# Kernel optimization log

Hardware: AMD Instinct MI355X
Metric: run time of the kernel (lower is better)

The kernel has to match this reference:

```python
import jax, jax.numpy as jnp
import numpy as np

T, B, OBS, H, FC = 128, 512, 1024, 512, 512
LN_EPS = 1e-6  # flax LayerNorm default


def setup_inputs() -> dict:
    key = jax.random.key(0)
    ks = jax.random.split(key, 8)
    sc = lambda k, shape, s: jax.random.normal(k, shape, jnp.float32) * s
    return dict(
        hidden=jnp.zeros((B, H), jnp.float32),  # GRUCell.initialize_carry -> zeros
        world_state=jax.random.normal(ks[0], (T, B, OBS), jnp.float32),
        dones=jax.random.bernoulli(ks[1], 0.05, (T, B)),
        Wd=sc(ks[2], (OBS, H), 1.0 / np.sqrt(OBS)),
        bd=jnp.zeros((H,), jnp.float32),
        ln_scale=jnp.ones((H,), jnp.float32),
        ln_bias=jnp.zeros((H,), jnp.float32),
        Wi=sc(ks[3], (H, 3 * H), 1.0 / np.sqrt(H)),  # input-side GRU weights [r|z|n]
        bi=jnp.zeros((3 * H,), jnp.float32),
        Wh=sc(ks[4], (H, 3 * H), 1.0 / np.sqrt(H)),  # hidden-side GRU weights [r|z|n]
        bhn=jnp.zeros((H,), jnp.float32),            # flax GRU: only hn dense has bias
        Wc1=sc(ks[5], (H, FC), 1.0 / np.sqrt(H)),
        bc1=jnp.zeros((FC,), jnp.float32),
        Wc2=sc(ks[6], (FC, 1), 1.0 / np.sqrt(FC)),
        bc2=jnp.zeros((1,), jnp.float32),
    )


def reference(hidden, world_state, dones, Wd, bd, ln_scale, ln_bias,
              Wi, bi, Wh, bhn, Wc1, bc1, Wc2, bc2):
    # Embed: Dense -> relu -> LayerNorm, applied to all timesteps at once
    emb = jax.nn.relu(world_state @ Wd + bd)                      # [T,B,H]
    mu = emb.mean(-1, keepdims=True)
    var = ((emb - mu) ** 2).mean(-1, keepdims=True)
    emb = (emb - mu) * jax.lax.rsqrt(var + LN_EPS) * ln_scale + ln_bias

    # Precompute input-side GRU projections for all steps (hoisted out of scan)
    xproj = emb @ Wi + bi                                         # [T,B,3H]

    def step(h, inputs):
        xp, done = inputs
        h = jnp.where(done[:, None], 0.0, h)                      # reset carry on done
        xr, xz, xn = jnp.split(xp, 3, axis=-1)
        hr, hz, hn = jnp.split(h @ Wh, 3, axis=-1)                # [B,H] each
        r = jax.nn.sigmoid(xr + hr)
        z = jax.nn.sigmoid(xz + hz)
        n = jnp.tanh(xn + r * (hn + bhn))
        h_new = (1.0 - z) * n + z * h
        return h_new, h_new

    h_last, ys = jax.lax.scan(step, hidden, (xproj, dones))       # ys: [T,B,H]

    critic = jax.nn.relu(ys @ Wc1 + bc1)                          # [T,B,FC]
    value = jnp.squeeze(critic @ Wc2 + bc2, axis=-1)              # [T,B]
    return h_last, value
```

## Files before the change

### kernel.cpp

```cpp
#include <hip/hip_runtime.h>
#include <stdint.h>

#define T_STEPS 128
#define BATCH   512
#define OBSD    1024
#define HD      512
#define FCD     512
#define MROWS   (T_STEPS * BATCH)

typedef unsigned short ushort_t;
typedef __attribute__((ext_vector_type(8))) short bf16x8;
typedef __attribute__((ext_vector_type(4))) float f32x4;
typedef __attribute__((ext_vector_type(2))) uint32_t u32x2;

__device__ inline ushort_t f2bf(float f) {
    union { float f; uint32_t u; } v; v.f = f;
    uint32_t r = v.u + 0x7FFFu + ((v.u >> 16) & 1u);
    return (ushort_t)(r >> 16);
}
__device__ inline float bf2f(ushort_t h) {
    union { uint32_t u; float f; } v; v.u = ((uint32_t)h) << 16;
    return v.f;
}
__device__ inline float fsigmoid(float x) {
    x = fminf(fmaxf(x, -30.f), 30.f);
    return 1.f / (1.f + __expf(-x));
}
__device__ inline float ftanh(float x) {
    float e = __expf(fminf(fmaxf(2.f * x, -30.f), 30.f));
    return (e - 1.f) / (e + 1.f);
}
__device__ inline uint32_t cvt_pk_bf16(float lo, float hi) {
    uint32_t r;
    asm("v_cvt_pk_bf16_f32 %0, %1, %2" : "=v"(r) : "v"(lo), "v"(hi));
    return r;
}
__device__ inline void gload16(const void* g, void* l) {
    __builtin_amdgcn_global_load_lds(
        (const __attribute__((address_space(1))) uint32_t*)g,
        (__attribute__((address_space(3))) uint32_t*)l, 16, 0, 0);
}

__global__ void transpose_to_bf16(const float* __restrict__ in,
                                  ushort_t* __restrict__ out, int R, int C) {
    __shared__ float tile[32][33];
    int tx = threadIdx.x, ty = threadIdx.y;
    int c0 = blockIdx.x * 32, r0 = blockIdx.y * 32;
    for (int yy = 0; yy < 4; ++yy)
        tile[ty + 8 * yy][tx] = in[(size_t)(r0 + ty + 8 * yy) * C + c0 + tx];
    __syncthreads();
    for (int yy = 0; yy < 4; ++yy)
        out[(size_t)(c0 + ty + 8 * yy) * R + r0 + tx] = f2bf(tile[tx][ty + 8 * yy]);
}

__global__ void init_misc(float* __restrict__ v, const float* __restrict__ bc2,
                          unsigned* __restrict__ bar) {
    int i = blockIdx.x * blockDim.x + threadIdx.x;
    if (i < MROWS) v[i] = bc2[0];
    if (i < 2048) bar[i] = 0u;
}

template <int K, int EPI, bool AF32>
__global__ __launch_bounds__(256, 2) void gemm128(
    const void* __restrict__ Aptr, const ushort_t* __restrict__ BT,
    const float* __restrict__ bias, ushort_t* __restrict__ Cout, int ldc,
    const float* __restrict__ wc2, float* __restrict__ value) {
    __shared__ __align__(16) ushort_t Als[128][32];
    __shared__ __align__(16) ushort_t Bls[128][32];
    int tid = threadIdx.x;
    int wave = tid >> 6, lane = tid & 63, quad = lane >> 4, l16 = lane & 15;
    int wr = wave >> 1, wc = wave & 1;
    int bm = blockIdx.y * 128, bn = blockIdx.x * 128;

    f32x4 acc[4][4];
#pragma unroll
    for (int m = 0; m < 4; ++m)
#pragma unroll
        for (int n = 0; n < 4; ++n) acc[m][n] = (f32x4){0.f, 0.f, 0.f, 0.f};

    int srow = tid >> 2;
    int sk = (tid & 3) * 8;
    const ushort_t* Bt0 = &BT[(size_t)(bn + srow) * K + sk];
    const ushort_t* Bt1 = &BT[(size_t)(bn + 64 + srow) * K + sk];
    char* AlsDst = (char*)&Als[0][0] + tid * 16;
    char* BlsDst = (char*)&Bls[0][0] + tid * 16;
    const ushort_t* At0 = nullptr;
    const ushort_t* At1 = nullptr;
    if constexpr (!AF32) {
        const ushort_t* A = (const ushort_t*)Aptr;
        At0 = &A[(size_t)(bm + srow) * K + sk];
        At1 = &A[(size_t)(bm + 64 + srow) * K + sk];
    }

#pragma unroll 1
    for (int k0 = 0; k0 < K; k0 += 32) {
        if constexpr (AF32) {
            const float* A = (const float*)Aptr;
#pragma unroll
            for (int j = 0; j < 4; ++j) {
                int f = tid + 256 * j;
                int r = f >> 3, c4 = f & 7;
                float4 av =
                    *(const float4*)&A[(size_t)(bm + r) * K + k0 + c4 * 4];
                u32x2 w;
                w[0] = cvt_pk_bf16(av.x, av.y);
                w[1] = cvt_pk_bf16(av.z, av.w);
                *(u32x2*)&Als[r][c4 * 4] = w;
            }
        } else {
            gload16(At0 + k0, AlsDst);
            gload16(At1 + k0, AlsDst + 4096);
        }
        gload16(Bt0 + k0, BlsDst);
        gload16(Bt1 + k0, BlsDst + 4096);
        __syncthreads();

        bf16x8 af[4], bfr[4];
#pragma unroll
        for (int m = 0; m < 4; ++m)
            af[m] = *(const bf16x8*)&Als[wr * 64 + m * 16 + l16][quad * 8];
#pragma unroll
        for (int n = 0; n < 4; ++n)
            bfr[n] = *(const bf16x8*)&Bls[wc * 64 + n * 16 + l16][quad * 8];
#pragma unroll
        for (int m = 0; m < 4; ++m)
#pragma unroll
            for (int n = 0; n < 4; ++n)
                acc[m][n] = __builtin_amdgcn_mfma_f32_16x16x32_bf16(
                    af[m], bfr[n], acc[m][n], 0, 0, 0);
        __syncthreads();
    }

    int rbase = bm + wr * 64 + quad * 4;
    if constexpr (EPI == 0 || EPI == 1) {
#pragma unroll
        for (int n = 0; n < 4; ++n) {
            int col = bn + wc * 64 + n * 16 + l16;
            float bv = bias[col];
#pragma unroll
            for (int m = 0; m < 4; ++m) {
#pragma unroll
                for (int i = 0; i < 4; ++i) {
                    float v = acc[m][n][i] + bv;
                    if constexpr (EPI == 0) v = fmaxf(v, 0.f);
                    Cout[(size_t)(rbase + m * 16 + i) * ldc + col] = f2bf(v);
                }
            }
        }
    } else {
        float s[4][4];
#pragma unroll
        for (int m = 0; m < 4; ++m)
#pragma unroll
            for (int i = 0; i < 4; ++i) s[m][i] = 0.f;
#pragma unroll
        for (int n = 0; n < 4; ++n) {
            int col = bn + wc * 64 + n * 16 + l16;
            float bv = bias[col], w2 = wc2[col];
#pragma unroll
            for (int m = 0; m < 4; ++m)
#pragma unroll
                for (int i = 0; i < 4; ++i)
                    s[m][i] += fmaxf(acc[m][n][i] + bv, 0.f) * w2;
        }
#pragma unroll
        for (int m = 0; m < 4; ++m)
#pragma unroll
            for (int i = 0; i < 4; ++i) {
                float v = s[m][i];
                v += __shfl_xor(v, 1);
                v += __shfl_xor(v, 2);
                v += __shfl_xor(v, 4);
                v += __shfl_xor(v, 8);
                if (l16 == 0) atomicAdd(&value[rbase + m * 16 + i], v);
            }
    }
}

__global__ __launch_bounds__(256) void ln_kernel(ushort_t* __restrict__ emb,
                                                 const float* __restrict__ scale,
                                                 const float* __restrict__ biasv) {
    int wave = threadIdx.x >> 6, lane = threadIdx.x & 63;
    size_t row = (size_t)blockIdx.x * 4 + wave;
    ushort_t* p = &emb[row * HD + lane * 8];
    bf16x8 xv = *(const bf16x8*)p;
    float x[8];
    float sum = 0.f, sq = 0.f;
    for (int j = 0; j < 8; ++j) {
        x[j] = bf2f((ushort_t)xv[j]);
        sum += x[j];
        sq += x[j] * x[j];
    }
    for (int off = 32; off > 0; off >>= 1) {
        sum += __shfl_xor(sum, off);
        sq += __shfl_xor(sq, off);
    }
    float mean = sum * (1.f / 512.f);
    float var = fmaxf(sq * (1.f / 512.f) - mean * mean, 0.f);
    float inv = rsqrtf(var + 1e-6f);
    bf16x8 ov;
    for (int j = 0; j < 8; ++j) {
        int col = lane * 8 + j;
        ov[j] = (short)f2bf((x[j] - mean) * inv * scale[col] + biasv[col]);
    }
    *(bf16x8*)p = ov;
}

__global__ __launch_bounds__(256, 1) void scan_coop(
    const float* __restrict__ hidden, const int* __restrict__ dones,
    const ushort_t* __restrict__ WhT, const float* __restrict__ bhn,
    const ushort_t* __restrict__ xproj, ushort_t* __restrict__ ys,
    float* __restrict__ hlast, ushort_t* hb0, ushort_t* hb1,
    unsigned* bar) {
    __shared__ __align__(16) ushort_t Wls[48][520];
    int tid = threadIdx.x;
    int wave = tid >> 6, lane = tid & 63, quad = lane >> 4, l16 = lane & 15;
    int bid = blockIdx.x;
    int bg = bid & 7, cg = bid >> 3;
    int row0 = bg * 64 + wave * 16;
    int col0 = cg * 16;

    for (int idx = tid; idx < 48 * 64; idx += 256) {
        int c = idx >> 6, ck = (idx & 63) * 8;
        int g = c >> 4, lc = c & 15;
        *(bf16x8*)&Wls[c][ck] =
            *(const bf16x8*)&WhT[(size_t)(g * 512 + col0 + lc) * 512 + ck];
    }

    float mast[4];
    int rbase = row0 + quad * 4;
#pragma unroll
    for (int i = 0; i < 4; ++i) {
        float h0 = hidden[(size_t)(rbase + i) * HD + col0 + l16];
        mast[i] = dones[rbase + i] ? 0.f : h0;
    }
    float bhnv = bhn[col0 + l16];

    unsigned* cnt = &bar[bg * 256];
    unsigned* mycnt = &cnt[(cg & 7) * 32];

#pragma unroll
    for (int i = 0; i < 4; ++i) {
        unsigned u = f2bf(mast[i]);
        unsigned p1 = __shfl_xor((int)u, 1);
        unsigned u32 = u | (p1 << 16);
        unsigned hi = __shfl_xor((int)u32, 2);
        if ((l16 & 3) == 0) {
            unsigned long long q =
                (unsigned long long)u32 | ((unsigned long long)hi << 32);
            __hip_atomic_store(
                (unsigned long long*)&hb0[(size_t)(rbase + i) * HD + col0 + l16],
                q, __ATOMIC_RELAXED, __HIP_MEMORY_SCOPE_AGENT);
        }
    }
    float xr[4], xz[4], xn[4];
    int dn_nxt[4];
#pragma unroll
    for (int i = 0; i < 4; ++i) {
        size_t m = (size_t)(rbase + i);
        const ushort_t* xp = &xproj[m * 1536 + col0 + l16];
        xr[i] = bf2f(xp[0]);
        xz[i] = bf2f(xp[512]);
        xn[i] = bf2f(xp[1024]);
        dn_nxt[i] = dones[BATCH + rbase + i];
    }
    __builtin_amdgcn_s_waitcnt(0);
    __syncthreads();
    if (tid == 0)
        __hip_atomic_fetch_add(mycnt, 1u, __ATOMIC_RELAXED,
                               __HIP_MEMORY_SCOPE_AGENT);

    for (int t = 0; t < T_STEPS; ++t) {
        if (tid == 0) {
            unsigned target = 32u * (unsigned)(t + 1);
            for (;;) {
                unsigned s = 0;
#pragma unroll
                for (int c = 0; c < 8; ++c)
                    s += __hip_atomic_load(&cnt[c * 32], __ATOMIC_RELAXED,
                                           __HIP_MEMORY_SCOPE_AGENT);
                if (s >= target) break;
                __builtin_amdgcn_s_sleep(1);
            }
        }
        __syncthreads();
        asm volatile("" ::: "memory");
        ushort_t* rbuf = (t & 1) ? hb1 : hb0;
        ushort_t* wnext = (t & 1) ? hb0 : hb1;

        bf16x8 afr[16];
        {
            const ushort_t* ap =
                &rbuf[(size_t)(row0 + l16) * HD + quad * 8];
            asm volatile(
                "global_load_dwordx4 %0, %16, off sc0 sc1\n\t"
                "global_load_dwordx4 %1, %16, off offset:64 sc0 sc1\n\t"
                "global_load_dwordx4 %2, %16, off offset:128 sc0 sc1\n\t"
                "global_load_dwordx4 %3, %16, off offset:192 sc0 sc1\n\t"
                "global_load_dwordx4 %4, %16, off offset:256 sc0 sc1\n\t"
                "global_load_dwordx4 %5, %16, off offset:320 sc0 sc1\n\t"
                "global_load_dwordx4 %6, %16, off offset:384 sc0 sc1\n\t"
                "global_load_dwordx4 %7, %16, off offset:448 sc0 sc1\n\t"
                "global_load_dwordx4 %8, %16, off offset:512 sc0 sc1\n\t"
                "global_load_dwordx4 %9, %16, off offset:576 sc0 sc1\n\t"
                "global_load_dwordx4 %10, %16, off offset:640 sc0 sc1\n\t"
                "global_load_dwordx4 %11, %16, off offset:704 sc0 sc1\n\t"
                "global_load_dwordx4 %12, %16, off offset:768 sc0 sc1\n\t"
                "global_load_dwordx4 %13, %16, off offset:832 sc0 sc1\n\t"
                "global_load_dwordx4 %14, %16, off offset:896 sc0 sc1\n\t"
                "global_load_dwordx4 %15, %16, off offset:960 sc0 sc1\n\t"
                "s_waitcnt vmcnt(0)"
                : "=&v"(afr[0]), "=&v"(afr[1]), "=&v"(afr[2]), "=&v"(afr[3]),
                  "=&v"(afr[4]), "=&v"(afr[5]), "=&v"(afr[6]), "=&v"(afr[7]),
                  "=&v"(afr[8]), "=&v"(afr[9]), "=&v"(afr[10]), "=&v"(afr[11]),
                  "=&v"(afr[12]), "=&v"(afr[13]), "=&v"(afr[14]), "=&v"(afr[15])
                : "v"(ap)
                : "memory");
        }
        f32x4 aR = (f32x4){0.f, 0.f, 0.f, 0.f};
        f32x4 aZ = (f32x4){0.f, 0.f, 0.f, 0.f};
        f32x4 aN = (f32x4){0.f, 0.f, 0.f, 0.f};
#pragma unroll
        for (int kt = 0; kt < 16; ++kt) {
            bf16x8 bR = *(const bf16x8*)&Wls[l16][kt * 32 + quad * 8];
            bf16x8 bZ = *(const bf16x8*)&Wls[16 + l16][kt * 32 + quad * 8];
            bf16x8 bN = *(const bf16x8*)&Wls[32 + l16][kt * 32 + quad * 8];
            aR = __builtin_amdgcn_mfma_f32_16x16x32_bf16(afr[kt], bR, aR, 0, 0, 0);
            aZ = __builtin_amdgcn_mfma_f32_16x16x32_bf16(afr[kt], bZ, aZ, 0, 0, 0);
            aN = __builtin_amdgcn_mfma_f32_16x16x32_bf16(afr[kt], bN, aN, 0, 0, 0);
        }

        unsigned long long qpk[4];
        float hnew[4];
#pragma unroll
        for (int i = 0; i < 4; ++i) {
            float r = fsigmoid(xr[i] + aR[i]);
            float z = fsigmoid(xz[i] + aZ[i]);
            float n = ftanh(xn[i] + r * (aN[i] + bhnv));
            hnew[i] = (1.f - z) * n + z * mast[i];
            unsigned u = f2bf(hnew[i]);
            unsigned p1 = __shfl_xor((int)u, 1);
            unsigned u32 = u | (p1 << 16);
            unsigned hi = __shfl_xor((int)u32, 2);
            qpk[i] = (unsigned long long)u32 | ((unsigned long long)hi << 32);
            mast[i] = (t < T_STEPS - 1 && dn_nxt[i]) ? 0.f : hnew[i];
        }
        if (t < T_STEPS - 1 && (l16 & 3) == 0) {
#pragma unroll
            for (int i = 0; i < 4; ++i) {
                unsigned long long qp = dn_nxt[i] ? 0ull : qpk[i];
                __hip_atomic_store(
                    (unsigned long long*)&wnext[(size_t)(rbase + i) * HD +
                                                col0 + l16],
                    qp, __ATOMIC_RELAXED, __HIP_MEMORY_SCOPE_AGENT);
            }
        }
        asm volatile("" ::: "memory");
        __builtin_amdgcn_s_waitcnt(0);
        if ((l16 & 3) == 0) {
#pragma unroll
            for (int i = 0; i < 4; ++i) {
                size_t m = (size_t)t * BATCH + rbase + i;
                *(unsigned long long*)&ys[m * HD + col0 + l16] = qpk[i];
            }
        }
        if (t < T_STEPS - 1) {
            int tn = t + 1;
            int td = (t + 2 < T_STEPS) ? t + 2 : T_STEPS - 1;
#pragma unroll
            for (int i = 0; i < 4; ++i) {
                size_t m = (size_t)tn * BATCH + rbase + i;
                const ushort_t* xp = &xproj[m * 1536 + col0 + l16];
                xr[i] = bf2f(xp[0]);
                xz[i] = bf2f(xp[512]);
                xn[i] = bf2f(xp[1024]);
                dn_nxt[i] = dones[td * BATCH + rbase + i];
            }
        }
        asm volatile("" ::: "memory");
        __syncthreads();
        if (tid == 0 && t < T_STEPS - 1)
            __hip_atomic_fetch_add(mycnt, 1u, __ATOMIC_RELAXED,
                                   __HIP_MEMORY_SCOPE_AGENT);
    }
#pragma unroll
    for (int i = 0; i < 4; ++i)
        hlast[(size_t)(rbase + i) * HD + col0 + l16] = mast[i];
}

extern "C" void kernel_launch(void* const* d_in, const int* in_sizes, int n_in,
                              void* d_out, int out_size, void* d_ws,
                              size_t ws_size, hipStream_t stream) {
    const float* hidden      = (const float*)d_in[0];
    const float* world_state = (const float*)d_in[1];
    const int*   dones       = (const int*)d_in[2];
    const float* Wd  = (const float*)d_in[3];
    const float* bd  = (const float*)d_in[4];
    const float* lns = (const float*)d_in[5];
    const float* lnb = (const float*)d_in[6];
    const float* Wi  = (const float*)d_in[7];
    const float* bi  = (const float*)d_in[8];
    const float* Wh  = (const float*)d_in[9];
    const float* bhn = (const float*)d_in[10];
    const float* Wc1 = (const float*)d_in[11];
    const float* bc1 = (const float*)d_in[12];
    const float* Wc2 = (const float*)d_in[13];
    const float* bc2 = (const float*)d_in[14];

    float* out_h = (float*)d_out;
    float* out_v = out_h + BATCH * HD;

    char* ws = (char*)d_ws;
    ushort_t* WdT   = (ushort_t*)(ws + 0);
    ushort_t* WiT   = (ushort_t*)(ws + 1048576);
    ushort_t* WhT   = (ushort_t*)(ws + 2621440);
    ushort_t* Wc1T  = (ushort_t*)(ws + 4194304);
    unsigned* bar   = (unsigned*)(ws + 4718592);
    ushort_t* hb0   = (ushort_t*)(ws + 4726784);
    ushort_t* hb1   = (ushort_t*)(ws + 5251072);
    ushort_t* xproj = (ushort_t*)(ws + 8388608);
    ushort_t* emb   = (ushort_t*)(ws + 209715200);
    ushort_t* ysb   = emb;

    dim3 tb(32, 8);
    transpose_to_bf16<<<dim3(16, 32), tb, 0, stream>>>(Wd, WdT, OBSD, HD);
    transpose_to_bf16<<<dim3(48, 16), tb, 0, stream>>>(Wi, WiT, HD, 1536);
    transpose_to_bf16<<<dim3(48, 16), tb, 0, stream>>>(Wh, WhT, HD, 1536);
    transpose_to_bf16<<<dim3(16, 16), tb, 0, stream>>>(Wc1, Wc1T, HD, FCD);
    init_misc<<<256, 256, 0, stream>>>(out_v, bc2, bar);

    gemm128<OBSD, 0, true><<<dim3(HD / 128, MROWS / 128), 256, 0, stream>>>(
        world_state, WdT, bd, emb, HD, nullptr, nullptr);
    ln_kernel<<<MROWS / 4, 256, 0, stream>>>(emb, lns, lnb);
    gemm128<HD, 1, false><<<dim3(1536 / 128, MROWS / 128), 256, 0, stream>>>(
        emb, WiT, bi, xproj, 1536, nullptr, nullptr);
    scan_coop<<<dim3(256), dim3(256), 0, stream>>>(
        hidden, dones, WhT, bhn, xproj, ysb, out_h, hb0, hb1, bar);
    gemm128<HD, 2, false><<<dim3(FCD / 128, MROWS / 128), 256, 0, stream>>>(
        ysb, Wc1T, bc1, nullptr, 0, Wc2, out_v);
}
```

Baseline: 1.428 ms.

## Replace block barrier with per-wave flag sync and keep Wh slice in registers

The scan kernel's grid barrier used per-block atomic counters, which needed __syncthreads and a single polling thread. It is replaced by per-wave flags that each wave sets after writing its 16 hidden rows. Each wave now waits only on the 32 column-group flags for its own 16 rows, polled by its lanes with a ballot, so no block-level barrier is needed. The Wh slice is also moved from LDS into registers (48 bf16x8 vectors per lane), which drops the LDS reads in the MFMA loop but raises register pressure.

```diff
diff --git a/kernel.cpp b/kernel.cpp
--- a/kernel.cpp
+++ b/kernel.cpp
@@ -212,7 +212,6 @@
     const ushort_t* __restrict__ xproj, ushort_t* __restrict__ ys,
     float* __restrict__ hlast, ushort_t* hb0, ushort_t* hb1,
     unsigned* bar) {
-    __shared__ __align__(16) ushort_t Wls[48][520];
     int tid = threadIdx.x;
     int wave = tid >> 6, lane = tid & 63, quad = lane >> 4, l16 = lane & 15;
     int bid = blockIdx.x;
@@ -220,11 +219,15 @@
     int row0 = bg * 64 + wave * 16;
     int col0 = cg * 16;
 
-    for (int idx = tid; idx < 48 * 64; idx += 256) {
-        int c = idx >> 6, ck = (idx & 63) * 8;
-        int g = c >> 4, lc = c & 15;
-        *(bf16x8*)&Wls[c][ck] =
-            *(const bf16x8*)&WhT[(size_t)(g * 512 + col0 + lc) * 512 + ck];
+    bf16x8 wR[16], wZ[16], wN[16];
+    {
+        const ushort_t* w0 = &WhT[(size_t)(col0 + l16) * 512 + quad * 8];
+#pragma unroll
+        for (int kt = 0; kt < 16; ++kt) {
+            wR[kt] = *(const bf16x8*)&w0[kt * 32];
+            wZ[kt] = *(const bf16x8*)&w0[262144 + kt * 32];
+            wN[kt] = *(const bf16x8*)&w0[524288 + kt * 32];
+        }
     }
 
     float mast[4];
@@ -236,8 +239,7 @@
     }
     float bhnv = bhn[col0 + l16];
 
-    unsigned* cnt = &bar[bg * 256];
-    unsigned* mycnt = &cnt[(cg & 7) * 32];
+    unsigned* flg = &bar[(unsigned)((bg * 4 + wave) * 32)];
 
 #pragma unroll
     for (int i = 0; i < 4; ++i) {
@@ -253,6 +255,10 @@
                 q, __ATOMIC_RELAXED, __HIP_MEMORY_SCOPE_AGENT);
         }
     }
+    asm volatile("s_waitcnt vmcnt(0)" ::: "memory");
+    if (lane == 0)
+        __hip_atomic_store(&flg[cg], 1u, __ATOMIC_RELAXED,
+                           __HIP_MEMORY_SCOPE_AGENT);
     float xr[4], xz[4], xn[4];
     int dn_nxt[4];
 #pragma unroll
@@ -264,26 +270,18 @@
         xn[i] = bf2f(xp[1024]);
         dn_nxt[i] = dones[BATCH + rbase + i];
     }
-    __builtin_amdgcn_s_waitcnt(0);
-    __syncthreads();
-    if (tid == 0)
-        __hip_atomic_fetch_add(mycnt, 1u, __ATOMIC_RELAXED,
-                               __HIP_MEMORY_SCOPE_AGENT);
+    asm volatile("" ::: "memory");
 
     for (int t = 0; t < T_STEPS; ++t) {
-        if (tid == 0) {
-            unsigned target = 32u * (unsigned)(t + 1);
+        {
+            unsigned tgt = (unsigned)(t + 1);
             for (;;) {
-                unsigned s = 0;
-#pragma unroll
-                for (int c = 0; c < 8; ++c)
-                    s += __hip_atomic_load(&cnt[c * 32], __ATOMIC_RELAXED,
-                                           __HIP_MEMORY_SCOPE_AGENT);
-                if (s >= target) break;
+                unsigned f = __hip_atomic_load(&flg[lane & 31], __ATOMIC_RELAXED,
+                                               __HIP_MEMORY_SCOPE_AGENT);
+                if (__ballot(f >= tgt) == ~0ull) break;
                 __builtin_amdgcn_s_sleep(1);
             }
         }
-        __syncthreads();
         asm volatile("" ::: "memory");
         ushort_t* rbuf = (t & 1) ? hb1 : hb0;
         ushort_t* wnext = (t & 1) ? hb0 : hb1;
@@ -322,12 +320,9 @@
         f32x4 aN = (f32x4){0.f, 0.f, 0.f, 0.f};
 #pragma unroll
         for (int kt = 0; kt < 16; ++kt) {
-            bf16x8 bR = *(const bf16x8*)&Wls[l16][kt * 32 + quad * 8];
-            bf16x8 bZ = *(const bf16x8*)&Wls[16 + l16][kt * 32 + quad * 8];
-            bf16x8 bN = *(const bf16x8*)&Wls[32 + l16][kt * 32 + quad * 8];
-            aR = __builtin_amdgcn_mfma_f32_16x16x32_bf16(afr[kt], bR, aR, 0, 0, 0);
-            aZ = __builtin_amdgcn_mfma_f32_16x16x32_bf16(afr[kt], bZ, aZ, 0, 0, 0);
-            aN = __builtin_amdgcn_mfma_f32_16x16x32_bf16(afr[kt], bN, aN, 0, 0, 0);
+            aR = __builtin_amdgcn_mfma_f32_16x16x32_bf16(afr[kt], wR[kt], aR, 0, 0, 0);
+            aZ = __builtin_amdgcn_mfma_f32_16x16x32_bf16(afr[kt], wZ[kt], aZ, 0, 0, 0);
+            aN = __builtin_amdgcn_mfma_f32_16x16x32_bf16(afr[kt], wN[kt], aN, 0, 0, 0);
         }
 
         unsigned long long qpk[4];
@@ -355,8 +350,11 @@
                     qp, __ATOMIC_RELAXED, __HIP_MEMORY_SCOPE_AGENT);
             }
         }
+        asm volatile("s_waitcnt vmcnt(0)" ::: "memory");
+        if (t < T_STEPS - 1 && lane == 0)
+            __hip_atomic_store(&flg[cg], (unsigned)(t + 2), __ATOMIC_RELAXED,
+                               __HIP_MEMORY_SCOPE_AGENT);
         asm volatile("" ::: "memory");
-        __builtin_amdgcn_s_waitcnt(0);
         if ((l16 & 3) == 0) {
 #pragma unroll
             for (int i = 0; i < 4; ++i) {
@@ -378,10 +376,6 @@
             }
         }
         asm volatile("" ::: "memory");
-        __syncthreads();
-        if (tid == 0 && t < T_STEPS - 1)
-            __hip_atomic_fetch_add(mycnt, 1u, __ATOMIC_RELAXED,
-                                   __HIP_MEMORY_SCOPE_AGENT);
     }
 #pragma unroll
     for (int i = 0; i < 4; ++i)
```

Result: no change. 1.415 ms (-0.9%).
